# Optimization experiments

Measured on AMD Instinct MI355X. Metric: run time of the kernel, lower is better.

Reference implementation:

```python
import jax, jax.numpy as jnp
import numpy as np

IN_CAPS = 1152
OUT_CAPS = 10
IN_DIM = 8
OUT_DIM = 16
ROUTING_ITERS = 3
BATCH = 512


def squash(s, axis=-1, eps=1e-8):
    # v = (||s||^2 / (1 + ||s||^2)) * s / ||s||
    mag_sq = jnp.sum(s * s, axis=axis, keepdims=True)
    mag = jnp.sqrt(mag_sq + eps)
    return (mag_sq / (1.0 + mag_sq)) * (s / mag)


def setup_inputs() -> dict:
    key = jax.random.key(0)
    kx, kw = jax.random.split(key)
    x = jax.random.normal(kx, (BATCH, IN_CAPS, IN_DIM), dtype=jnp.float32)
    stdv = 1.0 / np.sqrt(IN_CAPS)
    W = jax.random.uniform(kw, (IN_CAPS, OUT_CAPS, OUT_DIM, IN_DIM),
                           minval=-stdv, maxval=stdv, dtype=jnp.float32)
    return {"x": x, "W": W}


def reference(x, W):
    # u_hat[b,i,j,:] = W[i,j] @ x[b,i]  -> [B, 1152, 10, 16]
    u_hat = jnp.einsum('ijde,bie->bijd', W, x)
    u_det = jax.lax.stop_gradient(u_hat)
    b = jnp.zeros((x.shape[0], IN_CAPS, OUT_CAPS), dtype=x.dtype)
    v = None
    for it in range(ROUTING_ITERS):
        c = jax.nn.softmax(b, axis=2)  # softmax over out capsules
        u = u_hat if it == ROUTING_ITERS - 1 else u_det
        s = jnp.einsum('bij,bijd->bjd', c, u)  # [B, 10, 16]
        v = squash(s, axis=-1)
        if it != ROUTING_ITERS - 1:
            # agreement: u_hat . v  -> [B, 1152, 10]
            b = b + jnp.einsum('bijd,bjd->bij', u_det, v)
    return v  # [B, 10, 16]
```

## Files before the change

### kernel.cpp

```cpp
#include <hip/hip_runtime.h>
#include <math.h>

#define J 10
#define BT 16
#define NBT 32
#define NIC 16
#define ICB 72
#define IPW 18
#define JD 160
#define BATCH 512
#define IN_CAPS 1152
#define RTH 256

typedef __attribute__((ext_vector_type(8))) short short8;
typedef __attribute__((ext_vector_type(4))) float f32x4;
typedef __attribute__((ext_vector_type(4))) __fp16 fp16x4;
typedef __attribute__((ext_vector_type(2))) __fp16 fp16x2;

__device__ inline short f2bf(float f) {
    union { float f; unsigned u; } v; v.f = f;
    return (short)((v.u + 0x7FFFu + ((v.u >> 16) & 1u)) >> 16);
}
__device__ inline short8 cvt8(float4 a, float4 b) {
    short8 o;
    o[0] = f2bf(a.x); o[1] = f2bf(a.y); o[2] = f2bf(a.z); o[3] = f2bf(a.w);
    o[4] = f2bf(b.x); o[5] = f2bf(b.y); o[6] = f2bf(b.z); o[7] = f2bf(b.w);
    return o;
}

__global__ __launch_bounds__(256) void convert_w(
    const float* __restrict__ W, short* __restrict__ Wb, short* __restrict__ zb)
{
    const int t = blockIdx.x * 256 + threadIdx.x;
    const float4* src = (const float4*)W + (size_t)t * 2;
    *(short8*)(Wb + (size_t)t * 8) = cvt8(src[0], src[1]);
    if (blockIdx.x == 0 && threadIdx.x < 32) zb[threadIdx.x] = 0;
}

#define TI 32
#define TB 64
__global__ __launch_bounds__(256) void transpose_x(
    const float* __restrict__ X, short* __restrict__ Xb)
{
    __shared__ short8 tile[TI][TB + 1];
    const int it = blockIdx.x % (IN_CAPS / TI);
    const int bt = blockIdx.x / (IN_CAPS / TI);
    const int t  = threadIdx.x;

    const int i_l = t & 31, b_s = t >> 5;
#pragma unroll
    for (int p = 0; p < 8; ++p) {
        const int b_l = p * 8 + b_s;
        const float4* src = (const float4*)(X +
            (((size_t)(bt * TB + b_l)) * IN_CAPS + it * TI + i_l) * 8);
        tile[i_l][b_l] = cvt8(src[0], src[1]);
    }
    __syncthreads();
    const int b_l = t & 63, i_s = t >> 6;
#pragma unroll
    for (int p = 0; p < 8; ++p) {
        const int i_l2 = p * 4 + i_s;
        *(short8*)(Xb + (((size_t)(it * TI + i_l2)) * BATCH + bt * TB + b_l) * 8)
            = tile[i_l2][b_l];
    }
}

template<int MODE>
__global__ __launch_bounds__(RTH, 2) void route_kernel(
    const short* __restrict__ Xb, const short* __restrict__ Wb,
    const short* __restrict__ zb, const float* __restrict__ V,
    float* __restrict__ S_part)
{
    __shared__ float s_lds[BT][JD + 1];
    const int tid   = threadIdx.x;
    const int lane  = tid & 63, wave = tid >> 6;
    const int icb   = blockIdx.x % NIC;
    const int btile = blockIdx.x / NIC;
    const int bcol  = lane & 15, kg = lane >> 4;
    const int b     = btile * BT + bcol;

    for (int t = tid; t < BT * (JD + 1); t += RTH) (&s_lds[0][0])[t] = 0.f;
    __syncthreads();

    if (MODE == 0) {
        f32x4 acc[J];
#pragma unroll
        for (int j = 0; j < J; ++j) acc[j] = (f32x4)(0.f);
        for (int ks = wave; ks < ICB / 4; ks += 4) {
            const int ia = icb * ICB + ks * 4 + kg;
            const short8 bfr = *(const short8*)(Xb + ((size_t)ia * BATCH + b) * 8);
            short8 afr[J];
#pragma unroll
            for (int j = 0; j < J; ++j)
                afr[j] = *(const short8*)(Wb + (size_t)ia * 1280 + j * 128 + bcol * 8);
#pragma unroll
            for (int j = 0; j < J; ++j)
                acc[j] = __builtin_amdgcn_mfma_f32_16x16x32_bf16(afr[j], bfr, acc[j], 0, 0, 0);
        }
#pragma unroll
        for (int j = 0; j < J; ++j)
#pragma unroll
            for (int r = 0; r < 4; ++r)
                atomicAdd(&s_lds[bcol][j * 16 + kg * 4 + r], 0.1f * acc[j][r]);
    } else {
        float4 Vr[J];
#pragma unroll
        for (int j = 0; j < J; ++j)
            Vr[j] = *(const float4*)(V + (size_t)b * JD + j * 16 + kg * 4);

        float s_acc[J][4];
#pragma unroll
        for (int j = 0; j < J; ++j)
#pragma unroll
            for (int r = 0; r < 4; ++r) s_acc[j][r] = 0.f;

        fp16x4 ones;
        ones[0] = (__fp16)1.0f; ones[1] = (__fp16)1.0f;
        ones[2] = (__fp16)1.0f; ones[3] = (__fp16)1.0f;

        const int i0w = icb * ICB + wave * IPW;
        const short8 zero8 = (short8)(short)0;

#pragma unroll
        for (int g = 0; g < 5; ++g) {
            const int nt = (g < 4) ? 4 : 2;
            int ia = i0w + g * 4 + kg;
            if (ia > IN_CAPS - 1) ia = IN_CAPS - 1;

            short8 afr[J];
#pragma unroll
            for (int j = 0; j < J; ++j)
                afr[j] = *(const short8*)(Wb + (size_t)ia * 1280 + j * 128 + bcol * 8);
            const short8 bfull = *(const short8*)(Xb + ((size_t)ia * BATCH + b) * 8);

            for (int t = 0; t < nt; ++t) {
                const short8 bt = (kg == t) ? bfull : zero8;
                f32x4 u[J];
#pragma unroll
                for (int j = 0; j < J; ++j)
                    u[j] = __builtin_amdgcn_mfma_f32_16x16x32_bf16(afr[j], bt, (f32x4)(0.f), 0, 0, 0);

                float L[J];
#pragma unroll
                for (int j = 0; j < J; ++j) {
                    const float p0 = u[j][0] * Vr[j].x;
                    const float p1 = u[j][1] * Vr[j].y;
                    const float p2 = u[j][2] * Vr[j].z;
                    const float p3 = u[j][3] * Vr[j].w;
                    const fp16x2 a01 = __builtin_amdgcn_cvt_pkrtz(p0, p1);
                    const fp16x2 a23 = __builtin_amdgcn_cvt_pkrtz(p2, p3);
                    fp16x4 pb;
                    pb[0] = a01[0]; pb[1] = a01[1];
                    pb[2] = a23[0]; pb[3] = a23[1];
                    const f32x4 Lr = __builtin_amdgcn_mfma_f32_16x16x16f16(
                        ones, pb, (f32x4)(0.f), 0, 0, 0);
                    L[j] = Lr[0];
                }
                float c[J], Z = 0.f;
#pragma unroll
                for (int j = 0; j < J; ++j) { c[j] = __expf(L[j]); Z += c[j]; }
                const float rz = 1.0f / Z;
#pragma unroll
                for (int j = 0; j < J; ++j) {
                    const float cj = c[j] * rz;
                    s_acc[j][0] += cj * u[j][0];
                    s_acc[j][1] += cj * u[j][1];
                    s_acc[j][2] += cj * u[j][2];
                    s_acc[j][3] += cj * u[j][3];
                }
            }
        }
#pragma unroll
        for (int j = 0; j < J; ++j)
#pragma unroll
            for (int r = 0; r < 4; ++r)
                atomicAdd(&s_lds[bcol][j * 16 + kg * 4 + r], s_acc[j][r]);
    }
    __syncthreads();

    for (int t = tid; t < BT * JD; t += RTH) {
        const int bb = t / JD, p = t % JD;
        S_part[((size_t)icb * BATCH + btile * BT + bb) * JD + p] = s_lds[bb][p];
    }
}

__global__ __launch_bounds__(256) void squash_kernel(
    const float* __restrict__ S_part, float* __restrict__ V,
    float* __restrict__ out, int mode)
{
    const int t = blockIdx.x * 256 + threadIdx.x;
    float s = 0.f;
#pragma unroll
    for (int ic = 0; ic < NIC; ic++)
        s += S_part[(size_t)ic * BATCH * JD + t];
    float sq = s * s;
    sq += __shfl_xor(sq, 1);
    sq += __shfl_xor(sq, 2);
    sq += __shfl_xor(sq, 4);
    sq += __shfl_xor(sq, 8);
    const float v = s * sq / ((1.f + sq) * sqrtf(sq + 1e-8f));
    if (mode == 0)      V[t] = v;
    else if (mode == 1) V[t] += v;
    else                out[t] = v;
}

extern "C" void kernel_launch(void* const* d_in, const int* in_sizes, int n_in,
                              void* d_out, int out_size, void* d_ws, size_t ws_size,
                              hipStream_t stream)
{
    const float* X = (const float*)d_in[0];
    const float* W = (const float*)d_in[1];
    float* out = (float*)d_out;

    float* S_part = (float*)d_ws;
    float* V      = S_part + (size_t)NIC * BATCH * JD;
    short* Wb     = (short*)(V + (size_t)BATCH * JD);
    short* Xb     = Wb + (size_t)IN_CAPS * JD * 8;
    short* zb     = Xb + (size_t)IN_CAPS * BATCH * 8;

    const dim3 rg(NBT * NIC), rb(RTH);
    const dim3 sg(BATCH * JD / 256), sb(256);

    convert_w<<<dim3(720), dim3(256), 0, stream>>>(W, Wb, zb);
    transpose_x<<<dim3((IN_CAPS / TI) * (BATCH / TB)), dim3(256), 0, stream>>>(X, Xb);

    route_kernel<0><<<rg, rb, 0, stream>>>(Xb, Wb, zb, V, S_part);
    squash_kernel<<<sg, sb, 0, stream>>>(S_part, V, out, 0);
    route_kernel<1><<<rg, rb, 0, stream>>>(Xb, Wb, zb, V, S_part);
    squash_kernel<<<sg, sb, 0, stream>>>(S_part, V, out, 1);
    route_kernel<1><<<rg, rb, 0, stream>>>(Xb, Wb, zb, V, S_part);
    squash_kernel<<<sg, sb, 0, stream>>>(S_part, V, out, 2);
}
```

Before: 142.4 us.

## Fuse routing iterations and squash into one persistent kernel with group barriers

Replaces three route launches and three squash launches with a single 512-block kernel. Each group of 16 blocks sharing a batch tile synchronises through global atomic counters, so every block can reduce the partial sums itself and keep V in LDS. Partial sums ping-pong between two workspace buffers to avoid overwrite races. This removes launch overhead and the global round trips for V, but relies on all 512 blocks being co-resident (spin barrier) and adds redundant squash reduction work in every block.

```diff
diff --git a/kernel.cpp b/kernel.cpp
--- a/kernel.cpp
+++ b/kernel.cpp
@@ -11,6 +11,7 @@
 #define BATCH 512
 #define IN_CAPS 1152
 #define RTH 256
+#define VP 164
 
 typedef __attribute__((ext_vector_type(8))) short short8;
 typedef __attribute__((ext_vector_type(4))) float f32x4;
@@ -29,12 +30,11 @@
 }
 
 __global__ __launch_bounds__(256) void convert_w(
-    const float* __restrict__ W, short* __restrict__ Wb, short* __restrict__ zb)
+    const float* __restrict__ W, short* __restrict__ Wb)
 {
     const int t = blockIdx.x * 256 + threadIdx.x;
     const float4* src = (const float4*)W + (size_t)t * 2;
     *(short8*)(Wb + (size_t)t * 8) = cvt8(src[0], src[1]);
-    if (blockIdx.x == 0 && threadIdx.x < 32) zb[threadIdx.x] = 0;
 }
 
 #define TI 32
@@ -65,24 +65,44 @@
     }
 }
 
-template<int MODE>
-__global__ __launch_bounds__(RTH, 2) void route_kernel(
+__device__ inline void group_barrier(int* cnt, int g, int target)
+{
+    __syncthreads();
+    if (threadIdx.x == 0) {
+        __threadfence();
+        __hip_atomic_fetch_add(&cnt[g], 1, __ATOMIC_RELEASE,
+                               __HIP_MEMORY_SCOPE_AGENT);
+        while (__hip_atomic_load(&cnt[g], __ATOMIC_ACQUIRE,
+                                 __HIP_MEMORY_SCOPE_AGENT) < target) {}
+        __threadfence();
+    }
+    __syncthreads();
+}
+
+extern "C" __global__ void __launch_bounds__(RTH, 2) fused_route(
     const short* __restrict__ Xb, const short* __restrict__ Wb,
-    const short* __restrict__ zb, const float* __restrict__ V,
-    float* __restrict__ S_part)
+    float* __restrict__ S0, float* __restrict__ S1,
+    int* __restrict__ cnt, float* __restrict__ out)
 {
     __shared__ float s_lds[BT][JD + 1];
-    const int tid   = threadIdx.x;
-    const int lane  = tid & 63, wave = tid >> 6;
-    const int icb   = blockIdx.x % NIC;
-    const int btile = blockIdx.x / NIC;
-    const int bcol  = lane & 15, kg = lane >> 4;
-    const int b     = btile * BT + bcol;
+    __shared__ float V_lds[BT * VP];
+
+    const int tid  = threadIdx.x, bid = blockIdx.x;
+    const int lane = tid & 63, wave = tid >> 6;
+    const int xcd = bid & 7, slot = (bid >> 3) & 3, k = bid >> 5;
+    const int g = xcd * 4 + slot;
+    const int icb = k;
+    const int bcol = lane & 15, kg = lane >> 4;
+    const int b = g * BT + bcol;
+
+    fp16x4 ones;
+    ones[0] = (__fp16)1.0f; ones[1] = (__fp16)1.0f;
+    ones[2] = (__fp16)1.0f; ones[3] = (__fp16)1.0f;
+    const short8 zero8 = (short8)(short)0;
 
     for (int t = tid; t < BT * (JD + 1); t += RTH) (&s_lds[0][0])[t] = 0.f;
     __syncthreads();
-
-    if (MODE == 0) {
+    {
         f32x4 acc[J];
 #pragma unroll
         for (int j = 0; j < J; ++j) acc[j] = (f32x4)(0.f);
@@ -102,11 +122,42 @@
 #pragma unroll
             for (int r = 0; r < 4; ++r)
                 atomicAdd(&s_lds[bcol][j * 16 + kg * 4 + r], 0.1f * acc[j][r]);
-    } else {
+    }
+    __syncthreads();
+    for (int t = tid; t < BT * JD; t += RTH)
+        S0[((size_t)icb * BATCH + g * BT + t / JD) * JD + (t % JD)]
+            = (&s_lds[0][0])[(t / JD) * (JD + 1) + (t % JD)];
+
+    group_barrier(cnt, g, 16);
+
+#pragma unroll
+    for (int it = 0; it < 10; ++it) {
+        const int e = tid + it * 256;
+        const int bb = e / JD, p = e % JD;
+        float s = 0.f;
+#pragma unroll
+        for (int ic = 0; ic < NIC; ++ic)
+            s += S0[((size_t)ic * BATCH + g * BT + bb) * JD + p];
+        float sq = s * s;
+        sq += __shfl_xor(sq, 1);
+        sq += __shfl_xor(sq, 2);
+        sq += __shfl_xor(sq, 4);
+        sq += __shfl_xor(sq, 8);
+        V_lds[bb * VP + p] = s * sq / ((1.f + sq) * sqrtf(sq + 1e-8f));
+    }
+    __syncthreads();
+
+#pragma unroll 1
+    for (int iter = 1; iter <= 2; ++iter) {
+        float* Sw = (iter == 1) ? S1 : S0;
+
+        for (int t = tid; t < BT * (JD + 1); t += RTH) (&s_lds[0][0])[t] = 0.f;
+        __syncthreads();
+
         float4 Vr[J];
 #pragma unroll
         for (int j = 0; j < J; ++j)
-            Vr[j] = *(const float4*)(V + (size_t)b * JD + j * 16 + kg * 4);
+            Vr[j] = *(const float4*)&V_lds[bcol * VP + j * 16 + kg * 4];
 
         float s_acc[J][4];
 #pragma unroll
@@ -114,17 +165,12 @@
 #pragma unroll
             for (int r = 0; r < 4; ++r) s_acc[j][r] = 0.f;
 
-        fp16x4 ones;
-        ones[0] = (__fp16)1.0f; ones[1] = (__fp16)1.0f;
-        ones[2] = (__fp16)1.0f; ones[3] = (__fp16)1.0f;
-
         const int i0w = icb * ICB + wave * IPW;
-        const short8 zero8 = (short8)(short)0;
-
-#pragma unroll
-        for (int g = 0; g < 5; ++g) {
-            const int nt = (g < 4) ? 4 : 2;
-            int ia = i0w + g * 4 + kg;
+
+#pragma unroll
+        for (int gi = 0; gi < 5; ++gi) {
+            const int nt = (gi < 4) ? 4 : 2;
+            int ia = i0w + gi * 4 + kg;
             if (ia > IN_CAPS - 1) ia = IN_CAPS - 1;
 
             short8 afr[J];
@@ -175,33 +221,32 @@
 #pragma unroll
             for (int r = 0; r < 4; ++r)
                 atomicAdd(&s_lds[bcol][j * 16 + kg * 4 + r], s_acc[j][r]);
-    }
-    __syncthreads();
-
-    for (int t = tid; t < BT * JD; t += RTH) {
-        const int bb = t / JD, p = t % JD;
-        S_part[((size_t)icb * BATCH + btile * BT + bb) * JD + p] = s_lds[bb][p];
-    }
-}
-
-__global__ __launch_bounds__(256) void squash_kernel(
-    const float* __restrict__ S_part, float* __restrict__ V,
-    float* __restrict__ out, int mode)
-{
-    const int t = blockIdx.x * 256 + threadIdx.x;
-    float s = 0.f;
-#pragma unroll
-    for (int ic = 0; ic < NIC; ic++)
-        s += S_part[(size_t)ic * BATCH * JD + t];
-    float sq = s * s;
-    sq += __shfl_xor(sq, 1);
-    sq += __shfl_xor(sq, 2);
-    sq += __shfl_xor(sq, 4);
-    sq += __shfl_xor(sq, 8);
-    const float v = s * sq / ((1.f + sq) * sqrtf(sq + 1e-8f));
-    if (mode == 0)      V[t] = v;
-    else if (mode == 1) V[t] += v;
-    else                out[t] = v;
+        __syncthreads();
+        for (int t = tid; t < BT * JD; t += RTH)
+            Sw[((size_t)icb * BATCH + g * BT + t / JD) * JD + (t % JD)]
+                = (&s_lds[0][0])[(t / JD) * (JD + 1) + (t % JD)];
+
+        group_barrier(cnt, g, 16 * (iter + 1));
+
+#pragma unroll
+        for (int it2 = 0; it2 < 10; ++it2) {
+            const int e = tid + it2 * 256;
+            const int bb = e / JD, p = e % JD;
+            float s = 0.f;
+#pragma unroll
+            for (int ic = 0; ic < NIC; ++ic)
+                s += Sw[((size_t)ic * BATCH + g * BT + bb) * JD + p];
+            float sq = s * s;
+            sq += __shfl_xor(sq, 1);
+            sq += __shfl_xor(sq, 2);
+            sq += __shfl_xor(sq, 4);
+            sq += __shfl_xor(sq, 8);
+            const float v = s * sq / ((1.f + sq) * sqrtf(sq + 1e-8f));
+            if (iter == 1) V_lds[bb * VP + p] += v;
+            else if (k == 0) out[(g * BT + bb) * JD + p] = v;
+        }
+        __syncthreads();
+    }
 }
 
 extern "C" void kernel_launch(void* const* d_in, const int* in_sizes, int n_in,
@@ -212,22 +257,15 @@
     const float* W = (const float*)d_in[1];
     float* out = (float*)d_out;
 
-    float* S_part = (float*)d_ws;
-    float* V      = S_part + (size_t)NIC * BATCH * JD;
-    short* Wb     = (short*)(V + (size_t)BATCH * JD);
-    short* Xb     = Wb + (size_t)IN_CAPS * JD * 8;
-    short* zb     = Xb + (size_t)IN_CAPS * BATCH * 8;
-
-    const dim3 rg(NBT * NIC), rb(RTH);
-    const dim3 sg(BATCH * JD / 256), sb(256);
-
-    convert_w<<<dim3(720), dim3(256), 0, stream>>>(W, Wb, zb);
+    float* S0 = (float*)d_ws;
+    float* S1 = S0 + (size_t)NIC * BATCH * JD;
+    short* Wb = (short*)(S1 + (size_t)NIC * BATCH * JD);
+    short* Xb = Wb + (size_t)IN_CAPS * JD * 8;
+    int*   cnt = (int*)(Xb + (size_t)IN_CAPS * BATCH * 8);
+
+    (void)hipMemsetAsync(cnt, 0, 32 * sizeof(int), stream);
+    convert_w<<<dim3(720), dim3(256), 0, stream>>>(W, Wb);
     transpose_x<<<dim3((IN_CAPS / TI) * (BATCH / TB)), dim3(256), 0, stream>>>(X, Xb);
 
-    route_kernel<0><<<rg, rb, 0, stream>>>(Xb, Wb, zb, V, S_part);
-    squash_kernel<<<sg, sb, 0, stream>>>(S_part, V, out, 0);
-    route_kernel<1><<<rg, rb, 0, stream>>>(Xb, Wb, zb, V, S_part);
-    squash_kernel<<<sg, sb, 0, stream>>>(S_part, V, out, 1);
-    route_kernel<1><<<rg, rb, 0, stream>>>(Xb, Wb, zb, V, S_part);
-    squash_kernel<<<sg, sb, 0, stream>>>(S_part, V, out, 2);
-}
+    fused_route<<<dim3(512), dim3(RTH), 0, stream>>>(Xb, Wb, S0, S1, cnt, out);
+}
```

After: 540.9 us. +279.8%, slower.
